# Kernel tuning notes

Measured on AMD Instinct MI355X. Metric: run time of the kernel, lower is better.

The kernel has to match this reference:

```python
import jax, jax.numpy as jnp
import numpy as np

EPS = 1e-6

def poincare_pairwise_distance(x, c):
    """x: (B,N,E) points in Poincare ball, c: (C,E) centroids. Returns (B,N,C)."""
    x2 = jnp.sum(x * x, axis=-1)                  # (B,N)
    c2 = jnp.sum(c * c, axis=-1)                  # (C,)
    xc = jnp.einsum('bne,ce->bnc', x, c)          # (B,N,C)
    sq = jnp.maximum(x2[..., None] + c2[None, None, :] - 2.0 * xc, 0.0)  # ||x-c||^2
    den = (1.0 - x2)[..., None] * (1.0 - c2)[None, None, :]
    arg = 1.0 + 2.0 * sq / jnp.maximum(den, EPS)
    return jnp.arccosh(jnp.maximum(arg, 1.0 + EPS))

def setup_inputs() -> dict:
    key = jax.random.key(0)
    k1, k2 = jax.random.split(key)
    B, N, E, C = 32, 4096, 64, 256
    # scale so points lie strictly inside the unit ball (valid hyperbolic coords)
    node_repr = jax.random.normal(k1, (B, N, E), dtype=jnp.float32) * 0.05
    mask = jnp.ones((B, N, 1), dtype=jnp.float32)
    centroid = jax.random.normal(k2, (C, E), dtype=jnp.float32) * 0.01
    return {"node_repr": node_repr, "mask": mask, "centroid": centroid}

def reference(node_repr, mask, centroid):
    dist = poincare_pairwise_distance(node_repr, centroid)   # (B,N,C)
    dist = dist * mask                                       # mask: (B,N,1) broadcasts
    graph_dist = jnp.sum(dist, axis=1) / jnp.sum(mask, axis=1)  # (B,C)
    return graph_dist, dist
```

## Files before the change

### kernel.cpp

```cpp
#include <hip/hip_runtime.h>
#include <math.h>

#define E_DIM 64
#define C_DIM 256
#define EPS_F 1e-6f
#define LN2_F 0.69314718056f
#define TP    68

typedef __attribute__((ext_vector_type(8))) short short8;
typedef __attribute__((ext_vector_type(4))) float f32x4;

__device__ __forceinline__ unsigned short f2bf(float f) {
    unsigned int u = __float_as_uint(f);
    u += 0x7FFFu + ((u >> 16) & 1u);
    return (unsigned short)(u >> 16);
}

__device__ __forceinline__ short8 pack8(float4 a, float4 b) {
    short8 h;
    h[0] = (short)f2bf(a.x); h[1] = (short)f2bf(a.y);
    h[2] = (short)f2bf(a.z); h[3] = (short)f2bf(a.w);
    h[4] = (short)f2bf(b.x); h[5] = (short)f2bf(b.y);
    h[6] = (short)f2bf(b.z); h[7] = (short)f2bf(b.w);
    return h;
}

#define WS_F    0
#define WS_C2   32768
#define WS_RD2  33792
#define WS_INVM 34816

__global__ __launch_bounds__(C_DIM) void cdist_pre(
    const float* __restrict__ cent,
    const float* __restrict__ mask,
    unsigned char* __restrict__ ws,
    float* __restrict__ graph_acc,
    int N)
{
    const int t = threadIdx.x;
    if (blockIdx.x == 0) {
        float r[E_DIM];
        const float* cr = cent + t * E_DIM;
        #pragma unroll
        for (int e = 0; e < E_DIM; e += 4) {
            float4 v = *reinterpret_cast<const float4*>(cr + e);
            r[e] = v.x; r[e+1] = v.y; r[e+2] = v.z; r[e+3] = v.w;
        }
        float c2 = 0.f;
        #pragma unroll
        for (int e = 0; e < E_DIM; ++e) c2 = fmaf(r[e], r[e], c2);
        ((float*)(ws + WS_C2))[t]  = c2;
        ((float*)(ws + WS_RD2))[t] = 2.f / (1.f - c2);

        const int ct16 = t >> 4, l15 = t & 15;
        short8* F = (short8*)(ws + WS_F);
        #pragma unroll
        for (int kf = 0; kf < 2; ++kf) {
            #pragma unroll
            for (int q = 0; q < 4; ++q) {
                short8 h;
                #pragma unroll
                for (int j = 0; j < 8; ++j)
                    h[j] = (short)f2bf(r[kf * 32 + q * 8 + j]);
                F[(ct16 * 2 + kf) * 64 + 16 * q + l15] = h;
            }
        }
    } else {
        const int b = blockIdx.x - 1;
        graph_acc[b * C_DIM + t] = 0.f;
        float s = 0.f;
        for (int n = t; n < N; n += C_DIM) s += mask[(size_t)b * N + n];
        #pragma unroll
        for (int off = 32; off > 0; off >>= 1) s += __shfl_down(s, off, 64);
        __shared__ float partial[4];
        if ((t & 63) == 0) partial[t >> 6] = s;
        __syncthreads();
        if (t == 0) {
            float tot = partial[0] + partial[1] + partial[2] + partial[3];
            ((float*)(ws + WS_INVM))[b] = 1.f / tot;
        }
    }
}

template<int NT_TILES>
__global__ __launch_bounds__(256, 4) void cdist_mfma(
    const float* __restrict__ x,
    const float* __restrict__ mask,
    const unsigned char* __restrict__ ws,
    float*       __restrict__ graph_acc,
    float*       __restrict__ dist,
    int N)
{
    const int tid  = threadIdx.x;
    const int w    = tid >> 6;
    const int lane = tid & 63;
    const int l15  = lane & 15;
    const int q    = lane >> 4;
    const int n0   = blockIdx.x * (NT_TILES * 16);
    const int b    = blockIdx.y;

    __shared__ __align__(16) float sT[4][16 * TP];

    const short8* F    = (const short8*)(ws + WS_F);
    const float*  c2w  = (const float*)(ws + WS_C2);
    const float*  rd2w = (const float*)(ws + WS_RD2);

    short8 bfrag[4][2];
    #pragma unroll
    for (int ct = 0; ct < 4; ++ct)
        #pragma unroll
        for (int kf = 0; kf < 2; ++kf)
            bfrag[ct][kf] = F[((w * 4 + ct) * 2 + kf) * 64 + lane];

    float c2v[4], rd2v[4], gsum[4];
    #pragma unroll
    for (int ct = 0; ct < 4; ++ct) {
        const int c = w * 64 + ct * 16 + l15;
        c2v[ct] = c2w[c]; rd2v[ct] = rd2w[c]; gsum[ct] = 0.f;
    }

    const size_t rowbase = (size_t)b * N + n0;
    float* sW = sT[w];

    float4 pv0[2], pv1[2], pv2[2], pv3[2];
    float  pmk[2];
    {
        const float* xr0 = x + (rowbase + l15) * E_DIM + q * 8;
        pv0[0] = *reinterpret_cast<const float4*>(xr0);
        pv1[0] = *reinterpret_cast<const float4*>(xr0 + 4);
        pv2[0] = *reinterpret_cast<const float4*>(xr0 + 32);
        pv3[0] = *reinterpret_cast<const float4*>(xr0 + 36);
        pmk[0] = mask[rowbase + l15];
        const float* xr1 = xr0 + 16 * E_DIM;
        pv0[1] = *reinterpret_cast<const float4*>(xr1);
        pv1[1] = *reinterpret_cast<const float4*>(xr1 + 4);
        pv2[1] = *reinterpret_cast<const float4*>(xr1 + 32);
        pv3[1] = *reinterpret_cast<const float4*>(xr1 + 36);
        pmk[1] = mask[rowbase + 16 + l15];
    }

    #pragma unroll 2
    for (int rt = 0; rt < NT_TILES; ++rt) {
        const int s = rt & 1;
        const float4 u0 = pv0[s], u1 = pv1[s], u2 = pv2[s], u3 = pv3[s];
        const float  mkc = pmk[s];

        float ss = 0.f;
        ss = fmaf(u0.x, u0.x, ss); ss = fmaf(u0.y, u0.y, ss);
        ss = fmaf(u0.z, u0.z, ss); ss = fmaf(u0.w, u0.w, ss);
        ss = fmaf(u1.x, u1.x, ss); ss = fmaf(u1.y, u1.y, ss);
        ss = fmaf(u1.z, u1.z, ss); ss = fmaf(u1.w, u1.w, ss);
        ss = fmaf(u2.x, u2.x, ss); ss = fmaf(u2.y, u2.y, ss);
        ss = fmaf(u2.z, u2.z, ss); ss = fmaf(u2.w, u2.w, ss);
        ss = fmaf(u3.x, u3.x, ss); ss = fmaf(u3.y, u3.y, ss);
        ss = fmaf(u3.z, u3.z, ss); ss = fmaf(u3.w, u3.w, ss);
        ss += __shfl_xor(ss, 16);
        ss += __shfl_xor(ss, 32);

        const float rbrow = __builtin_amdgcn_rcpf(1.f - ss);
        const float krow  = LN2_F * mkc;

        short8 a0 = pack8(u0, u1);
        short8 a1 = pack8(u2, u3);

        if (rt + 2 < NT_TILES) {
            const float* xr = x + (rowbase + (rt + 2) * 16 + l15) * E_DIM + q * 8;
            pv0[s] = *reinterpret_cast<const float4*>(xr);
            pv1[s] = *reinterpret_cast<const float4*>(xr + 4);
            pv2[s] = *reinterpret_cast<const float4*>(xr + 32);
            pv3[s] = *reinterpret_cast<const float4*>(xr + 36);
            pmk[s] = mask[rowbase + (rt + 2) * 16 + l15];
        }

        f32x4 acc[4];
        #pragma unroll
        for (int ct = 0; ct < 4; ++ct) {
            f32x4 z = {0.f, 0.f, 0.f, 0.f};
            z = __builtin_amdgcn_mfma_f32_16x16x32_bf16(a0, bfrag[ct][0], z, 0, 0, 0);
            z = __builtin_amdgcn_mfma_f32_16x16x32_bf16(a1, bfrag[ct][1], z, 0, 0, 0);
            acc[ct] = z;
        }

        float ar[4], rbr[4], kr[4];
        #pragma unroll
        for (int reg = 0; reg < 4; ++reg) {
            const int src = q * 4 + reg;
            ar[reg]  = __shfl(ss,    src);
            rbr[reg] = __shfl(rbrow, src);
            kr[reg]  = __shfl(krow,  src);
        }

        #pragma unroll
        for (int ct = 0; ct < 4; ++ct) {
            #pragma unroll
            for (int reg = 0; reg < 4; ++reg) {
                const float dot = acc[ct][reg];
                float sq = fmaf(-2.f, dot, ar[reg] + c2v[ct]);
                sq = fmaxf(sq, 0.f);
                float uu = fmaxf(sq * (rbr[reg] * rd2v[ct]), EPS_F);
                float t  = uu + __builtin_amdgcn_sqrtf(fmaf(uu, uu, uu + uu));
                const float d = __builtin_amdgcn_logf(1.f + t) * kr[reg];
                sW[(q * 4 + reg) * TP + ct * 16 + l15] = d;
                gsum[ct] += d;
            }
        }

        #pragma unroll
        for (int i = 0; i < 4; ++i) {
            const int row2 = i * 4 + (lane >> 4);
            const int col2 = (lane & 15) * 4;
            f32x4 val = *reinterpret_cast<const f32x4*>(&sW[row2 * TP + col2]);
            __builtin_nontemporal_store(val, reinterpret_cast<f32x4*>(
                dist + (rowbase + rt * 16 + row2) * C_DIM + w * 64 + col2));
        }
    }

    const float inv = ((const float*)(ws + WS_INVM))[b];
    #pragma unroll
    for (int ct = 0; ct < 4; ++ct) {
        float s = gsum[ct];
        s += __shfl_xor(s, 16);
        s += __shfl_xor(s, 32);
        if (q == 0)
            atomicAdd(&graph_acc[b * C_DIM + w * 64 + ct * 16 + l15], s * inv);
    }
}

extern "C" void kernel_launch(void* const* d_in, const int* in_sizes, int n_in,
                              void* d_out, int out_size, void* d_ws, size_t ws_size,
                              hipStream_t stream) {
    const float* x    = (const float*)d_in[0];
    const float* mask = (const float*)d_in[1];
    const float* cent = (const float*)d_in[2];
    float* out = (float*)d_out;

    const long long BN = in_sizes[1];
    const int E = in_sizes[0] / (int)BN;
    const int C = in_sizes[2] / E;
    const int B = (int)(((long long)out_size - BN * C) / C);
    const int N = (int)(BN / B);

    float* graph_acc = out;
    float* dist_out  = out + (size_t)B * C;
    unsigned char* ws = (unsigned char*)d_ws;

    cdist_pre<<<dim3(B + 1), C_DIM, 0, stream>>>(cent, mask, ws, graph_acc, N);

    if (N % 128 == 0) {
        cdist_mfma<8><<<dim3(N / 128, B), 256, 0, stream>>>(
            x, mask, ws, graph_acc, dist_out, N);
    } else {
        cdist_mfma<4><<<dim3(N / 64, B), 256, 0, stream>>>(
            x, mask, ws, graph_acc, dist_out, N);
    }
}
```

Measured before the change: 214.0 us.

## Raise occupancy bound, split norm reduction, use plain stores and smaller tiles

```diff
diff --git a/kernel.cpp b/kernel.cpp
--- a/kernel.cpp
+++ b/kernel.cpp
@@ -83,7 +83,7 @@
 }
 
 template<int NT_TILES>
-__global__ __launch_bounds__(256, 4) void cdist_mfma(
+__global__ __launch_bounds__(256, 8) void cdist_mfma(
     const float* __restrict__ x,
     const float* __restrict__ mask,
     const unsigned char* __restrict__ ws,
@@ -145,15 +145,16 @@
         const float4 u0 = pv0[s], u1 = pv1[s], u2 = pv2[s], u3 = pv3[s];
         const float  mkc = pmk[s];
 
-        float ss = 0.f;
-        ss = fmaf(u0.x, u0.x, ss); ss = fmaf(u0.y, u0.y, ss);
-        ss = fmaf(u0.z, u0.z, ss); ss = fmaf(u0.w, u0.w, ss);
-        ss = fmaf(u1.x, u1.x, ss); ss = fmaf(u1.y, u1.y, ss);
-        ss = fmaf(u1.z, u1.z, ss); ss = fmaf(u1.w, u1.w, ss);
-        ss = fmaf(u2.x, u2.x, ss); ss = fmaf(u2.y, u2.y, ss);
-        ss = fmaf(u2.z, u2.z, ss); ss = fmaf(u2.w, u2.w, ss);
-        ss = fmaf(u3.x, u3.x, ss); ss = fmaf(u3.y, u3.y, ss);
-        ss = fmaf(u3.z, u3.z, ss); ss = fmaf(u3.w, u3.w, ss);
+        float sa = 0.f, sb = 0.f, sc = 0.f, sd = 0.f;
+        sa = fmaf(u0.x, u0.x, sa); sa = fmaf(u0.y, u0.y, sa);
+        sa = fmaf(u0.z, u0.z, sa); sa = fmaf(u0.w, u0.w, sa);
+        sb = fmaf(u1.x, u1.x, sb); sb = fmaf(u1.y, u1.y, sb);
+        sb = fmaf(u1.z, u1.z, sb); sb = fmaf(u1.w, u1.w, sb);
+        sc = fmaf(u2.x, u2.x, sc); sc = fmaf(u2.y, u2.y, sc);
+        sc = fmaf(u2.z, u2.z, sc); sc = fmaf(u2.w, u2.w, sc);
+        sd = fmaf(u3.x, u3.x, sd); sd = fmaf(u3.y, u3.y, sd);
+        sd = fmaf(u3.z, u3.z, sd); sd = fmaf(u3.w, u3.w, sd);
+        float ss = (sa + sb) + (sc + sd);
         ss += __shfl_xor(ss, 16);
         ss += __shfl_xor(ss, 32);
 
@@ -209,9 +210,9 @@
         for (int i = 0; i < 4; ++i) {
             const int row2 = i * 4 + (lane >> 4);
             const int col2 = (lane & 15) * 4;
-            f32x4 val = *reinterpret_cast<const f32x4*>(&sW[row2 * TP + col2]);
-            __builtin_nontemporal_store(val, reinterpret_cast<f32x4*>(
-                dist + (rowbase + rt * 16 + row2) * C_DIM + w * 64 + col2));
+            float4 val = *reinterpret_cast<const float4*>(&sW[row2 * TP + col2]);
+            *reinterpret_cast<float4*>(
+                dist + (rowbase + rt * 16 + row2) * C_DIM + w * 64 + col2) = val;
         }
     }
 
@@ -246,11 +247,6 @@
 
     cdist_pre<<<dim3(B + 1), C_DIM, 0, stream>>>(cent, mask, ws, graph_acc, N);
 
-    if (N % 128 == 0) {
-        cdist_mfma<8><<<dim3(N / 128, B), 256, 0, stream>>>(
-            x, mask, ws, graph_acc, dist_out, N);
-    } else {
-        cdist_mfma<4><<<dim3(N / 64, B), 256, 0, stream>>>(
-            x, mask, ws, graph_acc, dist_out, N);
-    }
-}
+    cdist_mfma<4><<<dim3(N / 64, B), 256, 0, stream>>>(
+        x, mask, ws, graph_acc, dist_out, N);
+}
```

Result: slower. 313.4 us (+46.4%).
